# Performance work log

Measured on AMD Instinct MI355X. Metric: run time of the kernel, lower is better.

Reference implementation:

```python
import jax, jax.numpy as jnp
import numpy as np

EPS = 1e-7
R = 3  # routing iterations


def conv(x, k, b, stride):
    y = jax.lax.conv_general_dilated(x, k, (stride, stride), 'VALID',
                                     dimension_numbers=('NHWC', 'HWIO', 'NHWC'))
    return y + b


def squash(s):
    n = jnp.linalg.norm(s, axis=-1, keepdims=True)
    return (n * n) / (1.0 + n * n) * s / (n + EPS)


def setup_inputs() -> dict:
    key = jax.random.key(0)
    ks = jax.random.split(key, 12)
    B = 256

    def g(k, shape, scale=0.05):
        return jax.random.normal(k, shape, dtype=jnp.float32) * scale

    return dict(
        x=jax.random.normal(ks[0], (B, 40, 40, 1), dtype=jnp.float32),
        y=jax.random.randint(ks[1], (B,), 0, 10),
        conv1_k=g(ks[2], (5, 5, 1, 64)),   conv1_b=jnp.zeros((64,), jnp.float32),
        conv2_k=g(ks[3], (9, 9, 64, 128)), conv2_b=jnp.zeros((128,), jnp.float32),
        conv3_k=g(ks[4], (9, 9, 128, 256)), conv3_b=jnp.zeros((256,), jnp.float32),
        prim_k=g(ks[5], (9, 9, 256, 256)), prim_b=jnp.zeros((256,), jnp.float32),
        w=g(ks[6], (1152, 10, 16, 8)),
        d1_w=g(ks[7], (160, 1024)),  d1_b=jnp.zeros((1024,), jnp.float32),
        d2_w=g(ks[8], (1024, 2048)), d2_b=jnp.zeros((2048,), jnp.float32),
        d3_w=g(ks[9], (2048, 1600)), d3_b=jnp.zeros((1600,), jnp.float32),
    )


def reference(x, y, conv1_k, conv1_b, conv2_k, conv2_b, conv3_k, conv3_b,
              prim_k, prim_b, w, d1_w, d1_b, d2_w, d2_b, d3_w, d3_b):
    # conv stack: 40 -> 36 -> 28 -> 20 -> 6 (primary caps, stride 2, linear)
    h = jax.nn.relu(conv(x, conv1_k, conv1_b, 1))
    h = jax.nn.relu(conv(h, conv2_k, conv2_b, 1))
    h = jax.nn.relu(conv(h, conv3_k, conv3_b, 1))
    h = conv(h, prim_k, prim_b, 2)                      # [B,6,6,256]
    B = h.shape[0]
    u = h.reshape(B, 1152, 8)                           # 1152 primary capsules of dim 8

    # pose predictions: u_hat[b,i,j,k] = sum_v w[i,j,k,v] * u[b,i,v]
    u_hat = jnp.einsum('ijkv,biv->bijk', w, u)          # [B,1152,10,16]

    # dynamic routing by agreement
    b_logit = jnp.zeros((B, 1152, 10), dtype=u_hat.dtype)
    for _ in range(R):
        c = jax.nn.softmax(b_logit, axis=2)[..., None]          # [B,1152,10,1]
        s = jnp.sum(c * u_hat, axis=1, keepdims=True)           # [B,1,10,16]
        v = squash(s)                                           # [B,1,10,16]
        b_logit = b_logit + jnp.sum(u_hat * v, axis=-1)         # agreement

    # masking by true label and reconstruction
    yh = jax.nn.one_hot(y, 10, dtype=v.dtype)                   # [B,10]
    v_masked = yh[:, None, :, None] * v                         # [B,1,10,16]
    v_flat = v_masked.reshape(B, 10 * 16)
    r1 = jax.nn.relu(v_flat @ d1_w + d1_b)
    r2 = jax.nn.relu(r1 @ d2_w + d2_b)
    recon = jax.nn.sigmoid(r2 @ d3_w + d3_b)                    # [B,1600]
    return (v, recon)
```

## Files before the change

### kernel.cpp

```cpp
#include <hip/hip_runtime.h>
#include <hip/hip_bf16.h>

typedef _Float16 f16;
typedef __attribute__((ext_vector_type(8))) _Float16 f16x8;
typedef __attribute__((ext_vector_type(4))) float f32x4;

__device__ __forceinline__ void gload_lds16(const void* g, void* l) {
  __builtin_amdgcn_global_load_lds((const __attribute__((address_space(1))) void*)g,
                                   (__attribute__((address_space(3))) void*)l, 16, 0, 0);
}

__device__ __forceinline__ void wtrans_body(const float* __restrict__ src,
                                            f16* __restrict__ dst,
                                            int K, int N, int k0, int n0) {
  __shared__ float tile[64][65];
  int t = threadIdx.x;
#pragma unroll
  for (int i = 0; i < 16; ++i) {
    int id = t + i * 256;
    int r = id >> 6, c = id & 63;
    tile[r][c] = (n0 + c < N) ? src[(size_t)(k0 + r) * N + n0 + c] : 0.f;
  }
  __syncthreads();
#pragma unroll
  for (int i = 0; i < 16; ++i) {
    int id = t + i * 256;
    int r = id >> 6, c = id & 63;
    dst[(size_t)(n0 + r) * K + k0 + c] = (f16)tile[c][r];
  }
}

__global__ __launch_bounds__(256) void wprepc_kernel(const float* __restrict__ s0, f16* __restrict__ d0,
                                                     const float* __restrict__ s1, f16* __restrict__ d1,
                                                     const float* __restrict__ s2, f16* __restrict__ d2) {
  int bid = (int)blockIdx.x;
  if (bid < 162) {
    int bx = bid % 81, by = bid / 81;
    wtrans_body(s0, d0, 5184, 128, bx * 64, by * 64);
  } else if (bid < 810) {
    int l = bid - 162; int bx = l % 162, by = l / 162;
    wtrans_body(s1, d1, 10368, 256, bx * 64, by * 64);
  } else {
    int l = bid - 810; int bx = l % 324, by = l / 324;
    wtrans_body(s2, d2, 20736, 256, bx * 64, by * 64);
  }
}

__global__ __launch_bounds__(256) void wprepd_kernel(const float* __restrict__ s0, f16* __restrict__ d0,
                                                     const float* __restrict__ s1, f16* __restrict__ d1) {
  int bid = (int)blockIdx.x;
  if (bid < 512) {
    int bx = bid % 16, by = bid / 16;
    wtrans_body(s0, d0, 1024, 2048, bx * 64, by * 64);
  } else {
    int l = bid - 512; int bx = l % 32, by = l / 32;
    wtrans_body(s1, d1, 2048, 1600, bx * 64, by * 64);
  }
}

__global__ __launch_bounds__(256) void conv1_kernel(const float* __restrict__ x,
                                                    const float* __restrict__ kw,
                                                    const float* __restrict__ bias,
                                                    f16* __restrict__ out) {
  int idx = blockIdx.x * 256 + threadIdx.x;
  int g = idx & 7;
  int co0 = g * 8;
  int r = idx >> 3;
  int ow = r % 36; int r2 = r / 36; int oh = r2 % 36; int b = r2 / 36;
  float acc[8];
#pragma unroll
  for (int j = 0; j < 8; ++j) acc[j] = bias[co0 + j];
  const float* xp = x + (b * 40 + oh) * 40 + ow;
#pragma unroll
  for (int dy = 0; dy < 5; ++dy)
#pragma unroll
    for (int dx = 0; dx < 5; ++dx) {
      float xv = xp[dy * 40 + dx];
      const float* kp = kw + (dy * 5 + dx) * 64 + co0;
#pragma unroll
      for (int j = 0; j < 8; ++j) acc[j] += xv * kp[j];
    }
  f16x8 o;
#pragma unroll
  for (int j = 0; j < 8; ++j) o[j] = (f16)fmaxf(acc[j], 0.f);
  *(f16x8*)(out + r * 64 + co0) = o;
}

template<int CIN, int WIN>
__device__ __forceinline__ int tapA_off(int kt) {
  int tap, ci0;
  if (CIN == 64)       { tap = kt;      ci0 = 0; }
  else if (CIN == 128) { tap = kt >> 1; ci0 = (kt & 1) << 6; }
  else                 { tap = kt >> 2; ci0 = (kt & 3) << 6; }
  int dy = tap / 9, dx = tap - dy * 9;
  return (dy * WIN + dx) * CIN + ci0;
}

template<int HIN, int WIN, int CIN, int HOUT, int WOUT, int COUT, int STRIDE,
         bool RELU, bool OUTF16>
__global__ __launch_bounds__(512, 2) void conv8p_kernel(const f16* __restrict__ in,
                                                        const f16* __restrict__ wt,
                                                        const float* __restrict__ bias,
                                                        f16* __restrict__ out16,
                                                        float* __restrict__ out32) {
  static_assert(COUT == 256, "BN=256 template requires COUT==256");
  constexpr int KTOT = 81 * CIN;
  constexpr int NT = KTOT / 64;
  __shared__ __align__(16) f16 lds[65536];
  const int mb = (int)blockIdx.x;
  const int t = threadIdx.x;
  const int wave = t >> 6, lane = t & 63;
  const int hi = lane >> 4, lo = lane & 15;
  const int wm = wave >> 2, wn = wave & 3;

  int Aoff[4], Boff[4];
  {
    int g = (lane & 7) ^ ((lane >> 3) & 7);
#pragma unroll
    for (int rbi = 0; rbi < 4; ++rbi) {
      int r = rbi * 64 + 8 * wave + (lane >> 3);
      int m = mb * 256 + r;
      int b = m / (HOUT * WOUT);
      int rr = m - b * (HOUT * WOUT);
      int oh = rr / WOUT, ow = rr - oh * WOUT;
      Aoff[rbi] = ((b * HIN + oh * STRIDE) * WIN + ow * STRIDE) * CIN + g * 8;
      Boff[rbi] = r * KTOT + g * 8;
    }
  }
  const int gb0 = (hi ^ (lo & 7)) << 4;
  const int gb1 = ((4 + hi) ^ (lo & 7)) << 4;

  const char* ldsc = (const char*)lds;
  char* ldsw = (char*)lds;

#define GA(rbi, tpo, bq) gload_lds16(in + Aoff[rbi] + (tpo),                        \
    (void*)(ldsw + (bq) * 32768 + ((rbi) * 64 + 8 * wave) * 128))
#define GB(rbi, tile) gload_lds16(wt + Boff[rbi] + ((tile) << 6),                   \
    (void*)(ldsw + 65536 + ((tile) & 1) * 32768 + ((rbi) * 64 + 8 * wave) * 128))

  {
    int tp0 = tapA_off<CIN, WIN>(0);
    GA(0, tp0, 0); GA(2, tp0, 0); GA(1, tp0, 0); GA(3, tp0, 0);
    GB(0, 0); GB(1, 0); GB(2, 0); GB(3, 0);
    GB(0, 1); GB(1, 1); GB(2, 1); GB(3, 1);
    asm volatile("s_waitcnt vmcnt(4)" ::: "memory");
    __builtin_amdgcn_s_barrier();
  }

  f32x4 acc[8][4] = {};

#define DO_PHASE(Q, STAGE)                                                          \
  {                                                                                 \
    f16x8 af[2][2];                                                                 \
    _Pragma("unroll")                                                               \
    for (int mf = 0; mf < 2; ++mf) {                                                \
      af[mf][0] = *(const f16x8*)(Ab + ((Q) * 2 + mf) * 2048 + gb0);                \
      af[mf][1] = *(const f16x8*)(Ab + ((Q) * 2 + mf) * 2048 + gb1);                \
    }                                                                               \
    STAGE;                                                                          \
    __builtin_amdgcn_s_barrier();                                                   \
    asm volatile("s_waitcnt lgkmcnt(0)" ::: "memory");                              \
    __builtin_amdgcn_sched_barrier(0);                                              \
    __builtin_amdgcn_s_setprio(1);                                                  \
    _Pragma("unroll")                                                               \
    for (int sb = 0; sb < 2; ++sb)                                                  \
      _Pragma("unroll")                                                             \
      for (int mf = 0; mf < 2; ++mf)                                                \
        _Pragma("unroll")                                                           \
        for (int nf = 0; nf < 4; ++nf)                                              \
          acc[(Q) * 2 + mf][nf] = __builtin_amdgcn_mfma_f32_16x16x32_f16(           \
              af[mf][sb], bfr[nf][sb], acc[(Q) * 2 + mf][nf], 0, 0, 0);             \
    __builtin_amdgcn_s_setprio(0);                                                  \
    __builtin_amdgcn_s_barrier();                                                   \
  }

  for (int T = 0; T < NT; ++T) {
    const int q = T & 1;
    const char* Ab = ldsc + q * 32768 + wm * 16384 + lo * 128;
    const char* Bb = ldsc + 65536 + q * 32768 + wn * 8192 + lo * 128;
    const int tpn = tapA_off<CIN, WIN>(T + 1);
    f16x8 bfr[4][2];
#pragma unroll
    for (int nf = 0; nf < 4; ++nf) {
      bfr[nf][0] = *(const f16x8*)(Bb + nf * 2048 + gb0);
      bfr[nf][1] = *(const f16x8*)(Bb + nf * 2048 + gb1);
    }
    DO_PHASE(0, if (T + 1 < NT) { GA(0, tpn, (T + 1) & 1); GA(2, tpn, (T + 1) & 1); })
    DO_PHASE(1, if (T + 1 < NT) { GA(1, tpn, (T + 1) & 1); GA(3, tpn, (T + 1) & 1); })
    DO_PHASE(2, if (T + 2 < NT) { GB(0, T + 2); GB(1, T + 2); })
    DO_PHASE(3,
      if (T + 2 < NT) {
        GB(2, T + 2); GB(3, T + 2);
        asm volatile("s_waitcnt vmcnt(4)" ::: "memory");
      } else {
        asm volatile("s_waitcnt vmcnt(0)" ::: "memory");
      })
  }
#undef DO_PHASE
#undef GA
#undef GB

#pragma unroll
  for (int mfr = 0; mfr < 8; ++mfr) {
#pragma unroll
    for (int nf = 0; nf < 4; ++nf) {
      int m0 = mb * 256 + wm * 128 + mfr * 16 + hi * 4;
      int n = wn * 64 + nf * 16 + lo;
      float bval = bias[n];
#pragma unroll
      for (int r = 0; r < 4; ++r) {
        float v = acc[mfr][nf][r] + bval;
        if (RELU) v = fmaxf(v, 0.f);
        int o = (m0 + r) * COUT + n;
        if (OUTF16) out16[o] = (f16)v; else out32[o] = v;
      }
    }
  }
}

template<int HIN, int WIN, int CIN, int HOUT, int WOUT, int COUT, int STRIDE,
         bool RELU, bool OUTF16, int SPLIT, bool ADDBIAS>
__global__ __launch_bounds__(256) void conv_mfma_kernel(const f16* __restrict__ in,
                                                        const f16* __restrict__ wt,
                                                        const float* __restrict__ bias,
                                                        f16* __restrict__ out16,
                                                        float* __restrict__ out32) {
  constexpr int KTOT = 81 * CIN;
  constexpr int NBLK = COUT / 128;
  constexpr int MTOT = 256 * HOUT * WOUT;
  constexpr int MBNB = (MTOT / 128) * NBLK;
  constexpr int NKT = (KTOT / 64) / SPLIT;
  __shared__ __align__(16) f16 lds[16384];
  int bidx = (int)blockIdx.x;
  int ks = 0;
  if (SPLIT > 1) { ks = bidx / MBNB; bidx -= ks * MBNB; }
  const int mb = bidx / NBLK;
  const int nb = bidx % NBLK;
  const int t = threadIdx.x;
  const int wave = t >> 6, lane = t & 63;
  const int hi = lane >> 4, lo = lane & 15;
  const bool isA = wave < 2;
  const int slot0 = wave << 9;

  int baseoff[8];
#pragma unroll
  for (int it = 0; it < 8; ++it) {
    int s = slot0 + it * 64 + lane;
    if (isA) {
      int row = s >> 3;
      int g = (s & 7) ^ (row & 7);
      int mg = mb * 128 + row;
      int b = mg / (HOUT * WOUT);
      int rr = mg - b * (HOUT * WOUT);
      int oh = rr / WOUT;
      int ow = rr - oh * WOUT;
      baseoff[it] = ((b * HIN + oh * STRIDE) * WIN + ow * STRIDE) * CIN + g * 8;
    } else {
      int sl = s - 1024;
      int row = sl >> 3;
      int g = (sl & 7) ^ (row & 7);
      baseoff[it] = (nb * 128 + row) * KTOT + g * 8;
    }
  }
  const f16* gsrc = isA ? in : wt;

  int aQ[4], bQ[4];
  const int wm = wave >> 1, wn = wave & 1;
#pragma unroll
  for (int f = 0; f < 4; ++f) {
    int arow = wm * 64 + f * 16 + lo;
    aQ[f] = (arow * 128) ^ ((arow & 7) << 4);
    int brow = wn * 64 + f * 16 + lo;
    bQ[f] = 16384 + ((brow * 128) ^ ((brow & 7) << 4));
  }

  f32x4 acc[4][4] = {};
  const char* ldsc = (const char*)lds;

  const int kt0 = ks * NKT;
  for (int kt = kt0; kt < kt0 + NKT; ++kt) {
    int tapoff;
    if (isA) tapoff = tapA_off<CIN, WIN>(kt);
    else     tapoff = kt << 6;
    __syncthreads();
#pragma unroll
    for (int it = 0; it < 8; ++it)
      gload_lds16(gsrc + baseoff[it] + tapoff,
                  (void*)((char*)lds + ((slot0 + it * 64) << 4)));
    __syncthreads();
#pragma unroll
    for (int sub = 0; sub < 2; ++sub) {
      const int gx = (sub * 4 + hi) << 4;
      f16x8 av[4], bv[4];
#pragma unroll
      for (int f = 0; f < 4; ++f) av[f] = *(const f16x8*)(ldsc + (aQ[f] ^ gx));
#pragma unroll
      for (int f = 0; f < 4; ++f) bv[f] = *(const f16x8*)(ldsc + (bQ[f] ^ gx));
#pragma unroll
      for (int mf = 0; mf < 4; ++mf)
#pragma unroll
        for (int nf = 0; nf < 4; ++nf)
          acc[mf][nf] = __builtin_amdgcn_mfma_f32_16x16x32_f16(av[mf], bv[nf],
                                                               acc[mf][nf], 0, 0, 0);
    }
  }

  float* o32 = out32 + (size_t)ks * MTOT * COUT;
#pragma unroll
  for (int mf = 0; mf < 4; ++mf) {
#pragma unroll
    for (int nf = 0; nf < 4; ++nf) {
      int m0 = mb * 128 + wm * 64 + mf * 16 + hi * 4;
      int n = nb * 128 + wn * 64 + nf * 16 + lo;
      float bval = ADDBIAS ? bias[n] : 0.f;
#pragma unroll
      for (int r = 0; r < 4; ++r) {
        float v = acc[mf][nf][r] + bval;
        if (RELU) v = fmaxf(v, 0.f);
        int o = (m0 + r) * COUT + n;
        if (OUTF16) out16[o] = (f16)v; else o32[o] = v;
      }
    }
  }
}

template<int K, int NP, int SPLIT>
__global__ __launch_bounds__(256) void gemm_mfma_kernel(const f16* __restrict__ A,
                                                        const f16* __restrict__ Bw,
                                                        float* __restrict__ dpart) {
  constexpr int NBLK = NP / 128;
  constexpr int MBNB = 2 * NBLK;
  constexpr int NKT = (K / 64) / SPLIT;
  __shared__ __align__(16) f16 lds[16384];
  int bidx = (int)blockIdx.x;
  int ks = 0;
  if (SPLIT > 1) { ks = bidx / MBNB; bidx -= ks * MBNB; }
  const int mb = bidx / NBLK;
  const int nb = bidx % NBLK;
  const int t = threadIdx.x;
  const int wave = t >> 6, lane = t & 63;
  const int hi = lane >> 4, lo = lane & 15;
  const bool isA = wave < 2;
  const int slot0 = wave << 9;

  int baseoff[8];
#pragma unroll
  for (int it = 0; it < 8; ++it) {
    int s = slot0 + it * 64 + lane;
    if (isA) {
      int row = s >> 3;
      int g = (s & 7) ^ (row & 7);
      baseoff[it] = (mb * 128 + row) * K + g * 8;
    } else {
      int sl = s - 1024;
      int row = sl >> 3;
      int g = (sl & 7) ^ (row & 7);
      baseoff[it] = (nb * 128 + row) * K + g * 8;
    }
  }
  const f16* gsrc = isA ? A : Bw;

  int aQ[4], bQ[4];
  const int wm = wave >> 1, wn = wave & 1;
#pragma unroll
  for (int f = 0; f < 4; ++f) {
    int arow = wm * 64 + f * 16 + lo;
    aQ[f] = (arow * 128) ^ ((arow & 7) << 4);
    int brow = wn * 64 + f * 16 + lo;
    bQ[f] = 16384 + ((brow * 128) ^ ((brow & 7) << 4));
  }

  f32x4 acc[4][4] = {};
  const char* ldsc = (const char*)lds;

  const int kt0 = ks * NKT;
  for (int kt = kt0; kt < kt0 + NKT; ++kt) {
    int tapoff = kt << 6;
    __syncthreads();
#pragma unroll
    for (int it = 0; it < 8; ++it)
      gload_lds16(gsrc + baseoff[it] + tapoff,
                  (void*)((char*)lds + ((slot0 + it * 64) << 4)));
    __syncthreads();
#pragma unroll
    for (int sub = 0; sub < 2; ++sub) {
      const int gx = (sub * 4 + hi) << 4;
      f16x8 av[4], bv[4];
#pragma unroll
      for (int f = 0; f < 4; ++f) av[f] = *(const f16x8*)(ldsc + (aQ[f] ^ gx));
#pragma unroll
      for (int f = 0; f < 4; ++f) bv[f] = *(const f16x8*)(ldsc + (bQ[f] ^ gx));
#pragma unroll
      for (int mf = 0; mf < 4; ++mf)
#pragma unroll
        for (int nf = 0; nf < 4; ++nf)
          acc[mf][nf] = __builtin_amdgcn_mfma_f32_16x16x32_f16(av[mf], bv[nf],
                                                               acc[mf][nf], 0, 0, 0);
    }
  }

  float* o32 = dpart + (size_t)ks * 256 * NP;
#pragma unroll
  for (int mf = 0; mf < 4; ++mf) {
#pragma unroll
    for (int nf = 0; nf < 4; ++nf) {
      int m0 = mb * 128 + wm * 64 + mf * 16 + hi * 4;
      int n = nb * 128 + wn * 64 + nf * 16 + lo;
#pragma unroll
      for (int r = 0; r < 4; ++r)
        o32[(m0 + r) * NP + n] = acc[mf][nf][r];
    }
  }
}

__global__ __launch_bounds__(256) void d2red_kernel(const float* __restrict__ part,
                                                    const float* __restrict__ bias,
                                                    f16* __restrict__ r2) {
  int idx = blockIdx.x * 256 + threadIdx.x;
  int e0 = idx * 4;
  int n0 = e0 & 2047;
  float4 a = *(const float4*)(part + e0);
  const float4 b1 = *(const float4*)(part + 524288 + e0);
  const float4 b2 = *(const float4*)(part + 1048576 + e0);
  const float4 b3 = *(const float4*)(part + 1572864 + e0);
  float v[4] = {a.x + b1.x + b2.x + b3.x, a.y + b1.y + b2.y + b3.y,
                a.z + b1.z + b2.z + b3.z, a.w + b1.w + b2.w + b3.w};
#pragma unroll
  for (int j = 0; j < 4; ++j)
    r2[e0 + j] = (f16)fmaxf(v[j] + bias[n0 + j], 0.f);
}

__global__ __launch_bounds__(256) void d3red_kernel(const float* __restrict__ part,
                                                    const float* __restrict__ bias,
                                                    float* __restrict__ recon) {
  int idx = blockIdx.x * 256 + threadIdx.x;
  int e0 = idx * 4;
  int n0 = e0 % 1664;
  int m = e0 / 1664;
  float v[4] = {0.f, 0.f, 0.f, 0.f};
#pragma unroll
  for (int s = 0; s < 8; ++s) {
    float4 a = *(const float4*)(part + s * 425984 + e0);
    v[0] += a.x; v[1] += a.y; v[2] += a.z; v[3] += a.w;
  }
#pragma unroll
  for (int j = 0; j < 4; ++j) {
    int n = n0 + j;
    if (n < 1600)
      recon[m * 1600 + n] = 1.f / (1.f + expf(-(v[j] + bias[n])));
  }
}

__global__ __launch_bounds__(320) void uhatps_kernel(const float* __restrict__ wf,
                                                     const float* __restrict__ part,
                                                     const float* __restrict__ pbias,
                                                     f16* __restrict__ uh,
                                                     float* __restrict__ parts) {
  __shared__ float pl[128][8];
  int blk = (int)blockIdx.x;
  int b = blk / 9, ic = blk - b * 9;
  int t = threadIdx.x;
  const int base = b * 9216 + ic * 1024;
  for (int e = t; e < 1024; e += 320) {
    float a = pbias[e & 255];
#pragma unroll
    for (int s = 0; s < 4; ++s) a += part[s * 2359296 + base + e];
    pl[e >> 3][e & 7] = a;
  }
  __syncthreads();
  int half = (t >= 160) ? 1 : 0;
  int jk = t - half * 160;
  int ibase = ic * 128 + half * 64;
  float sum = 0.f;
  for (int il = 0; il < 64; ++il) {
    int i = ibase + il;
    const float4* w4 = (const float4*)(wf + (i * 160 + jk) * 8);
    float4 w0 = w4[0], w1 = w4[1];
    const float* pr = pl[half * 64 + il];
    float acc = w0.x * pr[0] + w0.y * pr[1] + w0.z * pr[2] + w0.w * pr[3] +
                w1.x * pr[4] + w1.y * pr[5] + w1.z * pr[6] + w1.w * pr[7];
    uh[(b * 1152 + i) * 160 + jk] = (f16)acc;
    sum += acc;
  }
  parts[(b * 18 + ic * 2 + half) * 160 + jk] = sum;
}

template<int NCH, bool FIRST, bool WRITEB>
__global__ __launch_bounds__(256) void ba_kernel(const f16* __restrict__ uh,
                                                 const float* __restrict__ psrc,
                                                 float cscale,
                                                 float* __restrict__ blog,
                                                 float* __restrict__ pdst) {
  __shared__ f16 ul[128 * 172];
  __shared__ float vl[160];
  __shared__ float csm[128 * 10];
  int blk = (int)blockIdx.x;
  int b = blk / 9, ic = blk - b * 9;
  int t = threadIdx.x;
  const f16* ub = uh + (size_t)(b * 1152 + ic * 128) * 160;
  for (int e = t; e < 2560; e += 256) {
    int row = e / 20, col = e - row * 20;
    *(f16x8*)(ul + row * 172 + col * 8) = *(const f16x8*)(ub + row * 160 + col * 8);
  }
  if (t < 160) {
    float s = 0.f;
    for (int c = 0; c < NCH; ++c) s += psrc[(b * NCH + c) * 160 + t];
    s *= cscale;
    float ss = s * s;
    ss += __shfl_xor(ss, 1, 16);
    ss += __shfl_xor(ss, 2, 16);
    ss += __shfl_xor(ss, 4, 16);
    ss += __shfl_xor(ss, 8, 16);
    float n = sqrtf(ss);
    float f = ss / ((1.f + ss) * (n + 1e-7f));
    vl[t] = f * s;
  }
  __syncthreads();

  int il = t >> 1, half = t & 1, j0 = half * 5;
  const f16* ur = ul + il * 172 + j0 * 16;
  float agr[5];
#pragma unroll
  for (int j = 0; j < 5; ++j) {
    f16x8 a0 = *(const f16x8*)(ur + j * 16);
    f16x8 a1 = *(const f16x8*)(ur + j * 16 + 8);
    const float* vv = vl + (j0 + j) * 16;
    float s = (float)a0[0] * vv[0] + (float)a0[1] * vv[1] + (float)a0[2] * vv[2] +
              (float)a0[3] * vv[3] + (float)a0[4] * vv[4] + (float)a0[5] * vv[5] +
              (float)a0[6] * vv[6] + (float)a0[7] * vv[7] +
              (float)a1[0] * vv[8] + (float)a1[1] * vv[9] + (float)a1[2] * vv[10] +
              (float)a1[3] * vv[11] + (float)a1[4] * vv[12] + (float)a1[5] * vv[13] +
              (float)a1[6] * vv[14] + (float)a1[7] * vv[15];
    agr[j] = s;
  }
  int bbase = (b * 1152 + ic * 128 + il) * 10 + j0;
  float bl[5];
#pragma unroll
  for (int j = 0; j < 5; ++j) bl[j] = (FIRST ? 0.f : blog[bbase + j]) + agr[j];
  if (WRITEB) {
#pragma unroll
    for (int j = 0; j < 5; ++j) blog[bbase + j] = bl[j];
  }
  float mx = bl[0];
#pragma unroll
  for (int j = 1; j < 5; ++j) mx = fmaxf(mx, bl[j]);
  mx = fmaxf(mx, __shfl_xor(mx, 1));
  float e5[5], se = 0.f;
#pragma unroll
  for (int j = 0; j < 5; ++j) { e5[j] = expf(bl[j] - mx); se += e5[j]; }
  se += __shfl_xor(se, 1);
  float inv = 1.f / se;
#pragma unroll
  for (int j = 0; j < 5; ++j) csm[il * 10 + j0 + j] = e5[j] * inv;
  __syncthreads();

  if (t < 160) {
    int j = t >> 4;
    float s = 0.f;
    for (int il2 = 0; il2 < 128; ++il2)
      s += csm[il2 * 10 + j] * (float)ul[il2 * 172 + t];
    pdst[(b * 9 + ic) * 160 + t] = s;
  }
}

__global__ __launch_bounds__(1024) void maskd1v_kernel(const float* __restrict__ parts,
                                                       const int* __restrict__ y,
                                                       const float* __restrict__ w1,
                                                       const float* __restrict__ b1,
                                                       float* __restrict__ vout,
                                                       f16* __restrict__ r1) {
  __shared__ float vl[160];
  int b = blockIdx.x, t = threadIdx.x;
  if (t < 160) {
    float s = 0.f;
    for (int c = 0; c < 9; ++c) s += parts[(b * 9 + c) * 160 + t];
    float ss = s * s;
    ss += __shfl_xor(ss, 1, 16);
    ss += __shfl_xor(ss, 2, 16);
    ss += __shfl_xor(ss, 4, 16);
    ss += __shfl_xor(ss, 8, 16);
    float n = sqrtf(ss);
    float f = ss / ((1.f + ss) * (n + 1e-7f));
    float v = f * s;
    vl[t] = v;
    vout[b * 160 + t] = v;
  }
  __syncthreads();
  int yb = y[b];
  float acc = b1[t];
#pragma unroll
  for (int k = 0; k < 16; ++k) acc += vl[yb * 16 + k] * w1[(yb * 16 + k) * 1024 + t];
  r1[b * 1024 + t] = (f16)fmaxf(acc, 0.f);
}

extern "C" void kernel_launch(void* const* d_in, const int* in_sizes, int n_in,
                              void* d_out, int out_size, void* d_ws, size_t ws_size,
                              hipStream_t stream) {
  const float* x       = (const float*)d_in[0];
  const int*   y       = (const int*)d_in[1];
  const float* conv1_k = (const float*)d_in[2];
  const float* conv1_b = (const float*)d_in[3];
  const float* conv2_k = (const float*)d_in[4];
  const float* conv2_b = (const float*)d_in[5];
  const float* conv3_k = (const float*)d_in[6];
  const float* conv3_b = (const float*)d_in[7];
  const float* prim_k  = (const float*)d_in[8];
  const float* prim_b  = (const float*)d_in[9];
  const float* w_route = (const float*)d_in[10];
  const float* d1_w = (const float*)d_in[11];
  const float* d1_b = (const float*)d_in[12];
  const float* d2_w = (const float*)d_in[13];
  const float* d2_b = (const float*)d_in[14];
  const float* d3_w = (const float*)d_in[15];
  const float* d3_b = (const float*)d_in[16];

  char* ws = (char*)d_ws;
  f16*   h1      = (f16*)(ws + 0);
  float* part    = (float*)(ws + 0);
  float* dpart2  = (float*)(ws + 0);
  float* dpart3  = (float*)(ws + 16777216);
  f16*   h2      = (f16*)(ws + 42467328);
  f16*   uhat    = (f16*)(ws + 42467328);
  f16*   h3      = (f16*)(ws + 93847552);
  float* parts_a = (float*)(ws + 146276352);
  float* parts_b = (float*)(ws + 149225472);
  float* blog    = (float*)(ws + 155713536);
  f16*   r1h     = (f16*)(ws + 167673856);
  f16*   r2h     = (f16*)(ws + 168198144);
  f16*   wt2     = (f16*)(ws + 170819584);
  f16*   wt3     = (f16*)(ws + 172146688);
  f16*   wtp     = (f16*)(ws + 177455104);
  f16*   wd2     = (f16*)(ws + 177455104);
  f16*   wd3     = (f16*)(ws + 181649408);

  float* vout  = (float*)d_out;
  float* recon = (float*)d_out + 40960;

  wprepc_kernel<<<2106, 256, 0, stream>>>(conv2_k, wt2, conv3_k, wt3, prim_k, wtp);

  conv1_kernel<<<10368, 256, 0, stream>>>(x, conv1_k, conv1_b, h1);
  conv_mfma_kernel<36, 36, 64, 28, 28, 128, 1, true, true, 1, true>
      <<<1568, 256, 0, stream>>>(h1, wt2, conv2_b, h2, nullptr);
  conv8p_kernel<28, 28, 128, 20, 20, 256, 1, true, true>
      <<<400, 512, 0, stream>>>(h2, wt3, conv3_b, h3, nullptr);
  conv_mfma_kernel<20, 20, 256, 6, 6, 256, 2, false, false, 4, false>
      <<<576, 256, 0, stream>>>(h3, wtp, prim_b, nullptr, part);

  uhatps_kernel<<<2304, 320, 0, stream>>>(w_route, part, prim_b, uhat, parts_a);
  wprepd_kernel<<<1344, 256, 0, stream>>>(d2_w, wd2, d3_w, wd3);
  ba_kernel<18, true, true><<<2304, 256, 0, stream>>>(uhat, parts_a, 0.1f, blog, parts_b);
  ba_kernel<9, false, false><<<2304, 256, 0, stream>>>(uhat, parts_b, 1.0f, blog, parts_a);

  maskd1v_kernel<<<256, 1024, 0, stream>>>(parts_a, y, d1_w, d1_b, vout, r1h);
  gemm_mfma_kernel<1024, 2048, 4><<<128, 256, 0, stream>>>(r1h, wd2, dpart2);
  d2red_kernel<<<512, 256, 0, stream>>>(dpart2, d2_b, r2h);
  gemm_mfma_kernel<2048, 1664, 8><<<208, 256, 0, stream>>>(r2h, wd3, dpart3);
  d3red_kernel<<<416, 256, 0, stream>>>(dpart3, d3_b, recon);
}
```

Measured before the change: 1.226 ms.

## Split tail tiles of conv3 into K-thirds to balance final wave

The conv3 kernel had 400 blocks of 256 rows on a 256-CU device, leaving a ragged second wave. The first 256 tiles now run full-K as before, while the remaining 144 tiles are split into three K-slices, giving 688 blocks. Each slice writes f16 partial sums to workspace, and a new reduction kernel adds the three partials, the bias and the ReLU. This trades an extra launch, extra memory traffic and f16 rounding of the partial sums for better load balance across CUs.

```diff
diff --git a/kernel.cpp b/kernel.cpp
--- a/kernel.cpp
+++ b/kernel.cpp
@@ -97,17 +97,33 @@
 }
 
 template<int HIN, int WIN, int CIN, int HOUT, int WOUT, int COUT, int STRIDE,
-         bool RELU, bool OUTF16>
+         bool RELU, bool OUTF16, int FULLB, int TAILB>
 __global__ __launch_bounds__(512, 2) void conv8p_kernel(const f16* __restrict__ in,
                                                         const f16* __restrict__ wt,
                                                         const float* __restrict__ bias,
                                                         f16* __restrict__ out16,
-                                                        float* __restrict__ out32) {
+                                                        float* __restrict__ out32,
+                                                        f16* __restrict__ tp01,
+                                                        f16* __restrict__ tp2) {
   static_assert(COUT == 256, "BN=256 template requires COUT==256");
   constexpr int KTOT = 81 * CIN;
   constexpr int NT = KTOT / 64;
+  static_assert(TAILB == 0 || NT % 3 == 0, "K-third split requires NT%3==0");
+  constexpr int PNT = (TAILB > 0) ? NT / 3 : NT;
   __shared__ __align__(16) f16 lds[65536];
-  const int mb = (int)blockIdx.x;
+  const int bid = (int)blockIdx.x;
+  int mb, kt0, kt1;
+  f16* tp = nullptr;
+  if (TAILB == 0 || bid < FULLB) {
+    mb = bid; kt0 = 0; kt1 = NT;
+  } else {
+    int idx = bid - FULLB;
+    int piece = idx / TAILB;
+    int loc = idx - piece * TAILB;
+    mb = FULLB + loc;
+    kt0 = piece * PNT; kt1 = kt0 + PNT;
+    tp = (piece < 2 ? tp01 + (size_t)piece * TAILB * 65536 : tp2) + (size_t)loc * 65536;
+  }
   const int t = threadIdx.x;
   const int wave = t >> 6, lane = t & 63;
   const int hi = lane >> 4, lo = lane & 15;
@@ -139,10 +155,11 @@
     (void*)(ldsw + 65536 + ((tile) & 1) * 32768 + ((rbi) * 64 + 8 * wave) * 128))
 
   {
-    int tp0 = tapA_off<CIN, WIN>(0);
-    GA(0, tp0, 0); GA(2, tp0, 0); GA(1, tp0, 0); GA(3, tp0, 0);
-    GB(0, 0); GB(1, 0); GB(2, 0); GB(3, 0);
-    GB(0, 1); GB(1, 1); GB(2, 1); GB(3, 1);
+    int tq = tapA_off<CIN, WIN>(kt0);
+    int bq = kt0 & 1;
+    GA(0, tq, bq); GA(2, tq, bq); GA(1, tq, bq); GA(3, tq, bq);
+    GB(0, kt0); GB(1, kt0); GB(2, kt0); GB(3, kt0);
+    GB(0, kt0 + 1); GB(1, kt0 + 1); GB(2, kt0 + 1); GB(3, kt0 + 1);
     asm volatile("s_waitcnt vmcnt(4)" ::: "memory");
     __builtin_amdgcn_s_barrier();
   }
@@ -174,7 +191,7 @@
     __builtin_amdgcn_s_barrier();                                                   \
   }
 
-  for (int T = 0; T < NT; ++T) {
+  for (int T = kt0; T < kt1; ++T) {
     const int q = T & 1;
     const char* Ab = ldsc + q * 32768 + wm * 16384 + lo * 128;
     const char* Bb = ldsc + 65536 + q * 32768 + wn * 8192 + lo * 128;
@@ -185,11 +202,11 @@
       bfr[nf][0] = *(const f16x8*)(Bb + nf * 2048 + gb0);
       bfr[nf][1] = *(const f16x8*)(Bb + nf * 2048 + gb1);
     }
-    DO_PHASE(0, if (T + 1 < NT) { GA(0, tpn, (T + 1) & 1); GA(2, tpn, (T + 1) & 1); })
-    DO_PHASE(1, if (T + 1 < NT) { GA(1, tpn, (T + 1) & 1); GA(3, tpn, (T + 1) & 1); })
-    DO_PHASE(2, if (T + 2 < NT) { GB(0, T + 2); GB(1, T + 2); })
+    DO_PHASE(0, if (T + 1 < kt1) { GA(0, tpn, (T + 1) & 1); GA(2, tpn, (T + 1) & 1); })
+    DO_PHASE(1, if (T + 1 < kt1) { GA(1, tpn, (T + 1) & 1); GA(3, tpn, (T + 1) & 1); })
+    DO_PHASE(2, if (T + 2 < kt1) { GB(0, T + 2); GB(1, T + 2); })
     DO_PHASE(3,
-      if (T + 2 < NT) {
+      if (T + 2 < kt1) {
         GB(2, T + 2); GB(3, T + 2);
         asm volatile("s_waitcnt vmcnt(4)" ::: "memory");
       } else {
@@ -200,22 +217,55 @@
 #undef GA
 #undef GB
 
-#pragma unroll
-  for (int mfr = 0; mfr < 8; ++mfr) {
-#pragma unroll
-    for (int nf = 0; nf < 4; ++nf) {
-      int m0 = mb * 256 + wm * 128 + mfr * 16 + hi * 4;
-      int n = wn * 64 + nf * 16 + lo;
-      float bval = bias[n];
-#pragma unroll
-      for (int r = 0; r < 4; ++r) {
-        float v = acc[mfr][nf][r] + bval;
-        if (RELU) v = fmaxf(v, 0.f);
-        int o = (m0 + r) * COUT + n;
-        if (OUTF16) out16[o] = (f16)v; else out32[o] = v;
+  if (tp == nullptr) {
+#pragma unroll
+    for (int mfr = 0; mfr < 8; ++mfr) {
+#pragma unroll
+      for (int nf = 0; nf < 4; ++nf) {
+        int m0 = mb * 256 + wm * 128 + mfr * 16 + hi * 4;
+        int n = wn * 64 + nf * 16 + lo;
+        float bval = bias[n];
+#pragma unroll
+        for (int r = 0; r < 4; ++r) {
+          float v = acc[mfr][nf][r] + bval;
+          if (RELU) v = fmaxf(v, 0.f);
+          int o = (m0 + r) * COUT + n;
+          if (OUTF16) out16[o] = (f16)v; else out32[o] = v;
+        }
       }
     }
-  }
+  } else {
+#pragma unroll
+    for (int mfr = 0; mfr < 8; ++mfr) {
+#pragma unroll
+      for (int nf = 0; nf < 4; ++nf) {
+        int rowloc = wm * 128 + mfr * 16 + hi * 4;
+        int n = wn * 64 + nf * 16 + lo;
+#pragma unroll
+        for (int r = 0; r < 4; ++r)
+          tp[(rowloc + r) * 256 + n] = (f16)acc[mfr][nf][r];
+      }
+    }
+  }
+}
+
+__global__ __launch_bounds__(256) void tailred3_kernel(const f16* __restrict__ tp01,
+                                                       const f16* __restrict__ tp2,
+                                                       const float* __restrict__ bias,
+                                                       f16* __restrict__ h3) {
+  int idx = blockIdx.x * 256 + threadIdx.x;
+  int e0 = idx * 8;
+  int n0 = e0 & 255;
+  f16x8 a = *(const f16x8*)(tp01 + e0);
+  f16x8 b = *(const f16x8*)(tp01 + 9437184 + e0);
+  f16x8 c = *(const f16x8*)(tp2 + e0);
+  f16x8 o;
+#pragma unroll
+  for (int j = 0; j < 8; ++j) {
+    float v = (float)a[j] + (float)b[j] + (float)c[j] + bias[n0 + j];
+    o[j] = (f16)fmaxf(v, 0.f);
+  }
+  *(f16x8*)(h3 + 16777216 + e0) = o;
 }
 
 template<int HIN, int WIN, int CIN, int HOUT, int WOUT, int COUT, int STRIDE,
@@ -616,12 +666,14 @@
 
   char* ws = (char*)d_ws;
   f16*   h1      = (f16*)(ws + 0);
+  f16*   tpart01 = (f16*)(ws + 0);
   float* part    = (float*)(ws + 0);
   float* dpart2  = (float*)(ws + 0);
   float* dpart3  = (float*)(ws + 16777216);
   f16*   h2      = (f16*)(ws + 42467328);
   f16*   uhat    = (f16*)(ws + 42467328);
   f16*   h3      = (f16*)(ws + 93847552);
+  f16*   tpart2  = (f16*)(ws + 146276352);
   float* parts_a = (float*)(ws + 146276352);
   float* parts_b = (float*)(ws + 149225472);
   float* blog    = (float*)(ws + 155713536);
@@ -641,8 +693,9 @@
   conv1_kernel<<<10368, 256, 0, stream>>>(x, conv1_k, conv1_b, h1);
   conv_mfma_kernel<36, 36, 64, 28, 28, 128, 1, true, true, 1, true>
       <<<1568, 256, 0, stream>>>(h1, wt2, conv2_b, h2, nullptr);
-  conv8p_kernel<28, 28, 128, 20, 20, 256, 1, true, true>
-      <<<400, 512, 0, stream>>>(h2, wt3, conv3_b, h3, nullptr);
+  conv8p_kernel<28, 28, 128, 20, 20, 256, 1, true, true, 256, 144>
+      <<<688, 512, 0, stream>>>(h2, wt3, conv3_b, h3, nullptr, tpart01, tpart2);
+  tailred3_kernel<<<4608, 256, 0, stream>>>(tpart01, tpart2, conv3_b, h3);
   conv_mfma_kernel<20, 20, 256, 6, 6, 256, 2, false, false, 4, false>
       <<<576, 256, 0, stream>>>(h3, wtp, prim_b, nullptr, part);
 
```

After: 1.201 ms. 2.0% less time.
